# Kernel optimization log

Hardware: AMD Instinct MI355X
Metric: run time of the kernel (lower is better)

The kernel has to match this reference:

```python
import jax, jax.numpy as jnp
import numpy as np
from jax import lax

# --- static config (mirrors cfg / init args) ---
B, T, F_IN = 4, 1024, 80      # batch, time steps, mel bins (80 -> freq collapses to 1)
C_EMB = 512                   # cfg.dim_embed
C0 = C_EMB // 2               # first_conv_filters (non-tcn branch)
HEADS, K = 8, 7               # num_heads, NA kernel_size (dilation=1)
D_HEAD = C_EMB // HEADS
MLP = 4 * C_EMB               # mlp_ratio=4
EPS = 1e-5                    # layer_norm_eps


def setup_inputs() -> dict:
    key = jax.random.key(0)
    ks = jax.random.split(key, 16)
    rn = lambda k, s, sc=0.02: jax.random.normal(k, s, dtype=jnp.float32) * sc
    z = lambda *s: jnp.zeros(s, dtype=jnp.float32)
    o = lambda *s: jnp.ones(s, dtype=jnp.float32)
    return {
        "x": jax.random.normal(ks[0], (B, 1, T, F_IN), dtype=jnp.float32),
        # conv embedding stack (OIHW)
        "conv0_w": rn(ks[1], (C0, 1, 3, 3), 0.1), "conv0_b": z(C0),
        "conv1_w": rn(ks[2], (C_EMB, C0, 1, 12), 0.02), "conv1_b": z(C_EMB),
        "conv2_w": rn(ks[3], (C_EMB, C_EMB, 3, 3), 0.02), "conv2_b": z(C_EMB),
        "emb_ln_g": o(C_EMB), "emb_ln_b": z(C_EMB),
        # neighborhood attention (linear weights stored [in,out]; apply as x @ W + b)
        "q_w": rn(ks[4], (C_EMB, C_EMB)), "q_b": z(C_EMB),
        "k_w": rn(ks[5], (C_EMB, C_EMB)), "k_b": z(C_EMB),
        "v_w": rn(ks[6], (C_EMB, C_EMB)), "v_b": z(C_EMB),
        "rpb": rn(ks[7], (HEADS, 2 * K - 1)),
        "attn_out_w": rn(ks[8], (C_EMB, C_EMB)), "attn_out_b": z(C_EMB),
        "ln1_g": o(C_EMB), "ln1_b": z(C_EMB),
        "ln2_g": o(C_EMB), "ln2_b": z(C_EMB),
        "mlp1_w": rn(ks[9], (C_EMB, MLP)), "mlp1_b": z(MLP),
        "mlp2_w": rn(ks[10], (MLP, C_EMB)), "mlp2_b": z(C_EMB),
    }


def _layer_norm(x, g, b):
    m = jnp.mean(x, axis=-1, keepdims=True)
    v = jnp.mean(jnp.square(x - m), axis=-1, keepdims=True)
    return (x - m) * lax.rsqrt(v + EPS) * g + b


def _na1d(q, k, v, rpb):
    """1D neighborhood attention (natten1dqkrpb + softmax + natten1dav), dilation=1.
    q,k,v: [B,H,T,D]; rpb: [H,2K-1]. Returns [B,H,T,D]."""
    Bq, H, Tq, D = q.shape
    ni = jnp.clip(jnp.arange(Tq) - K // 2, 0, Tq - K)        # window start per query
    idx = ni[:, None] + jnp.arange(K)                         # [T,K] key positions
    k_win = k[:, :, idx]                                      # [B,H,T,K,D]
    v_win = v[:, :, idx]                                      # [B,H,T,K,D]
    scores = jnp.einsum('bhtd,bhtkd->bhtk', q, k_win)
    rel = idx - jnp.arange(Tq)[:, None] + (K - 1)             # [T,K] in [0,2K-2]
    scores = scores + rpb[:, rel][None]                       # + [1,H,T,K]
    probs = jax.nn.softmax(scores, axis=-1)
    return jnp.einsum('bhtk,bhtkd->bhtd', probs, v_win)


def _forward(x, conv0_w, conv0_b, conv1_w, conv1_b, conv2_w, conv2_b,
             emb_ln_g, emb_ln_b, q_w, q_b, k_w, k_b, v_w, v_b, rpb,
             attn_out_w, attn_out_b, ln1_g, ln1_b, ln2_g, ln2_b,
             mlp1_w, mlp1_b, mlp2_w, mlp2_b):
    conv = lambda h, w, b, pad: lax.conv_general_dilated(
        h, w, (1, 1), pad, dimension_numbers=('NCHW', 'OIHW', 'NCHW')
    ) + b[None, :, None, None]
    pool3 = lambda h: lax.reduce_window(h, -jnp.inf, lax.max,
                                        (1, 1, 1, 3), (1, 1, 1, 3), 'VALID')
    # --- AllInOneEmbeddings (eval: dropouts are no-ops) ---
    h = jax.nn.relu(pool3(conv(x, conv0_w, conv0_b, [(1, 1), (0, 0)])))
    h = jax.nn.relu(pool3(conv(h, conv1_w, conv1_b, [(0, 0), (0, 0)])))
    h = jax.nn.relu(pool3(conv(h, conv2_w, conv2_b, [(1, 1), (0, 0)])))
    h = jnp.transpose(h[..., 0], (0, 2, 1))                   # [B,T,C]
    emb = _layer_norm(h, emb_ln_g, emb_ln_b)
    # --- DinatLayer1d (double_attention=False, drop_path=0) ---
    Bh, Th, Ch = emb.shape
    shortcut = emb
    hs = _layer_norm(emb, ln1_g, ln1_b)
    heads = lambda y: jnp.transpose(y.reshape(Bh, Th, HEADS, D_HEAD), (0, 2, 1, 3))
    q = heads(hs @ q_w + q_b) * (1.0 / jnp.sqrt(jnp.float32(D_HEAD)))
    kk = heads(hs @ k_w + k_b)
    vv = heads(hs @ v_w + v_b)
    ctx = _na1d(q, kk, vv, rpb)                               # [B,H,T,D]
    ctx = jnp.transpose(ctx, (0, 2, 1, 3)).reshape(Bh, Th, Ch)
    attn = ctx @ attn_out_w + attn_out_b                      # NeighborhoodAttentionOutput
    hs = shortcut + attn
    ln = _layer_norm(hs, ln2_g, ln2_b)
    mlp = jax.nn.gelu(ln @ mlp1_w + mlp1_b, approximate=False) @ mlp2_w + mlp2_b
    return hs + mlp


def reference(x, conv0_w, conv0_b, conv1_w, conv1_b, conv2_w, conv2_b,
              emb_ln_g, emb_ln_b, q_w, q_b, k_w, k_b, v_w, v_b, rpb,
              attn_out_w, attn_out_b, ln1_g, ln1_b, ln2_g, ln2_b,
              mlp1_w, mlp1_b, mlp2_w, mlp2_b):
    return _forward(x, conv0_w, conv0_b, conv1_w, conv1_b, conv2_w, conv2_b,
                    emb_ln_g, emb_ln_b, q_w, q_b, k_w, k_b, v_w, v_b, rpb,
                    attn_out_w, attn_out_b, ln1_g, ln1_b, ln2_g, ln2_b,
                    mlp1_w, mlp1_b, mlp2_w, mlp2_b)
```

## Files before the change

kernel.cpp:

```cpp
#include <hip/hip_runtime.h>
#include <hip/hip_bf16.h>
#include <math.h>


typedef __bf16 bf16x8 __attribute__((ext_vector_type(8)));
typedef float f32x4 __attribute__((ext_vector_type(4)));

static __device__ __forceinline__ short f2bf(float f) {
  __hip_bfloat16 h = __float2bfloat16(f);
  return __builtin_bit_cast(short, h);
}

static __device__ __forceinline__ float wave_sum(float v) {
#pragma unroll
  for (int o = 32; o; o >>= 1) v += __shfl_xor(v, o);
  return v;
}

static __device__ __forceinline__ void gld16(const void* g, void* l) {
  __builtin_amdgcn_global_load_lds(
      (const __attribute__((address_space(1))) unsigned int*)g,
      (__attribute__((address_space(3))) unsigned int*)l, 16, 0, 0);
}

__global__ __launch_bounds__(256) void conv0_kernel(
    const float* __restrict__ x, const float* __restrict__ w,
    const float* __restrict__ bias, short* __restrict__ h0) {
  const int b = blockIdx.x >> 10;
  const int t = blockIdx.x & 1023;
  const int c = threadIdx.x;
  __shared__ float xs[3][80];
  for (int i = threadIdx.x; i < 240; i += 256) {
    int dt = i / 80, f = i - dt * 80;
    int tt = t + dt - 1;
    xs[dt][f] = (tt >= 0 && tt < 1024) ? x[(b * 1024 + tt) * 80 + f] : 0.f;
  }
  float wr[9];
#pragma unroll
  for (int i = 0; i < 9; ++i) wr[i] = w[c * 9 + i];
  const float bi = bias[c];
  __syncthreads();
  const int cc = c >> 5, q = (c >> 3) & 3, e = c & 7;
  short* outb = &h0[((size_t)(b * 8 + cc) * 1024 + t) * 896];
  for (int fo = 0; fo < 26; ++fo) {
    float m = -1e30f;
#pragma unroll
    for (int p = 0; p < 3; ++p) {
      const int f = fo * 3 + p;
      float acc = bi;
#pragma unroll
      for (int dt = 0; dt < 3; ++dt)
#pragma unroll
        for (int df = 0; df < 3; ++df)
          acc += xs[dt][f + df] * wr[dt * 3 + df];
      m = fmaxf(m, acc);
    }
    const int row = t * 28 + fo;
    outb[fo * 32 + (q ^ ((row >> 1) & 3)) * 8 + e] = f2bf(fmaxf(m, 0.f));
  }
  if (c < 64) outb[832 + c] = 0;
}

__global__ __launch_bounds__(256) void prep_w1(const float* __restrict__ w,
                                               short* __restrict__ wt) {
  const int co = blockIdx.x;
  __shared__ float ls[3072];
  for (int i = threadIdx.x; i < 3072; i += 256) ls[i] = w[co * 3072 + i];
  __syncthreads();
  const int swz = (co >> 1) & 3;
  for (int i = threadIdx.x; i < 3072; i += 256) {
    const int e = i & 7, q = (i >> 3) & 3, kw = (i >> 5) % 12, cc = i / 384;
    const int ci = cc * 32 + q * 8 + e;
    wt[(((size_t)(cc * 12 + kw) * 512 + co) * 4 + (q ^ swz)) * 8 + e] =
        f2bf(ls[ci * 12 + kw]);
  }
}

__global__ __launch_bounds__(256) void prep_w2(const float* __restrict__ w,
                                               short* __restrict__ wt) {
  const int co = blockIdx.x;
  __shared__ float ls[4608];
  for (int i = threadIdx.x; i < 4608; i += 256) ls[i] = w[co * 4608 + i];
  __syncthreads();
  const int swz = (co >> 1) & 3;
  for (int i = threadIdx.x; i < 4608; i += 256) {
    const int e = i & 7, q = (i >> 3) & 3, p = (i >> 5) % 9, cc = i / 288;
    const int ci = cc * 32 + q * 8 + e;
    wt[(((size_t)(cc * 9 + p) * 512 + co) * 4 + (q ^ swz)) * 8 + e] =
        f2bf(ls[ci * 9 + p]);
  }
}

__global__ void prep_wt(const float* __restrict__ w, short* __restrict__ wt,
                        int K, int N) {
  __shared__ float tile[32][33];
  const int k0 = blockIdx.x * 32, n0 = blockIdx.y * 32;
  const int tx = threadIdx.x, ty = threadIdx.y;
  for (int r = ty; r < 32; r += 8) tile[r][tx] = w[(size_t)(k0 + r) * N + n0 + tx];
  __syncthreads();
  for (int r = ty; r < 32; r += 8) wt[(size_t)(n0 + r) * K + k0 + tx] = f2bf(tile[tx][r]);
}

__global__ __launch_bounds__(256) void zero_h1_edges(short* __restrict__ h1) {
  short* base = h1 + (size_t)blockIdx.x * 164160;
  for (int i = threadIdx.x; i < 160; i += 256) {
    base[i] = 0;
    base[1025 * 160 + i] = 0;
  }
}

__global__ __launch_bounds__(512) void conv1_kernel(
    const short* __restrict__ h0, const short* __restrict__ wt1,
    const float* __restrict__ bias, short* __restrict__ h1) {
  const int b = blockIdx.x >> 5;
  const int t0 = (blockIdx.x & 31) * 32;
  const int co0 = blockIdx.y * 128;
  __shared__ short XsF[2][28672];
  __shared__ short AsF[2][8192];
  const int tid = threadIdx.x;
  const int lane = tid & 63;
  const int wid = tid >> 6;
  const int wm = wid >> 2;
  const int wn = wid & 3;
  const int l15 = lane & 15, lg = lane >> 4;

  const f32x4 zf = {0.f, 0.f, 0.f, 0.f};
  f32x4 acc[4][8];
#pragma unroll
  for (int i = 0; i < 4; ++i)
#pragma unroll
    for (int j = 0; j < 8; ++j) acc[i][j] = zf;

  auto stageX = [&](int cc, int buf) {
    const short* xs = h0 + ((size_t)(b * 8 + cc) * 1024 + t0) * 896;
#pragma unroll
    for (int i = 0; i < 7; ++i) {
      const int v = wid * 7 + i;
      gld16(xs + v * 512 + lane * 8, &XsF[buf][v * 512]);
    }
  };
  auto stageA = [&](int cc, int g, int buf) {
#pragma unroll
    for (int i = 0; i < 2; ++i) {
      const int u = wid * 2 + i;
      const int kwl = u >> 3, r = u & 7;
      gld16(wt1 + ((size_t)((cc * 12 + g * 2 + kwl) * 512) + co0) * 32 +
                r * 512 + lane * 8,
            &AsF[buf][kwl * 4096 + r * 512]);
    }
  };

  stageX(0, 0);
  stageA(0, 0, 0);
  asm volatile("s_waitcnt vmcnt(0)" ::: "memory");
  __builtin_amdgcn_s_barrier();

  for (int s = 0; s < 48; ++s) {
    const int cc = s / 6, g = s - cc * 6;
    if (s < 47) {
      const int s1 = s + 1;
      const int cc1 = s1 / 6, g1 = s1 - cc1 * 6;
      stageA(cc1, g1, s1 & 1);
      if (g1 == 0) {
        stageX(cc1, cc1 & 1);
        asm volatile("s_waitcnt vmcnt(9)" ::: "memory");
      } else {
        asm volatile("s_waitcnt vmcnt(2)" ::: "memory");
      }
    } else {
      asm volatile("s_waitcnt vmcnt(0)" ::: "memory");
    }
    __builtin_amdgcn_s_barrier();
    const short* Xb = XsF[cc & 1];
    const short* Ab = AsF[s & 1];
#pragma unroll
    for (int j = 0; j < 2; ++j) {
      const int kw = g * 2 + j;
      bf16x8 a[4];
#pragma unroll
      for (int sm = 0; sm < 4; ++sm) {
        const int co_l = wm * 64 + sm * 16 + l15;
        a[sm] = *reinterpret_cast<const bf16x8*>(
            &Ab[(j * 512 + co_l * 4 + (lg ^ ((co_l >> 1) & 3))) * 8]);
      }
#pragma unroll
      for (int sn = 0; sn < 8; ++sn) {
        const int row = (wn * 8 + sn) * 28 + l15 + kw;
        bf16x8 bf = *reinterpret_cast<const bf16x8*>(
            &Xb[(row * 4 + (lg ^ ((row >> 1) & 3))) * 8]);
#pragma unroll
        for (int sm = 0; sm < 4; ++sm)
          acc[sm][sn] = __builtin_amdgcn_mfma_f32_16x16x32_bf16(a[sm], bf, acc[sm][sn], 0, 0, 0);
      }
    }
    asm volatile("" ::: "memory");
    __builtin_amdgcn_s_barrier();
  }
  const int basel = lane & 48;
  const int wsrc = (l15 < 5) ? 3 * l15 : 0;
#pragma unroll
  for (int sm = 0; sm < 4; ++sm)
#pragma unroll
    for (int sn = 0; sn < 8; ++sn) {
      const int t = t0 + wn * 8 + sn;
#pragma unroll
      for (int r = 0; r < 4; ++r) {
        float val = acc[sm][sn][r];
        float v0 = __shfl(val, basel + wsrc);
        float v1 = __shfl(val, basel + wsrc + 1);
        float v2 = __shfl(val, basel + wsrc + 2);
        if (l15 < 5) {
          const int co = co0 + wm * 64 + sm * 16 + lg * 4 + r;
          float p = fmaxf(fmaxf(v0, v1), v2) + bias[co];
          const int cc2 = co >> 5, q = (co >> 3) & 3, e = co & 7;
          const int row_g = (t + 1) * 5 + l15;
          h1[((size_t)(b * 16 + cc2) * 1026 + (t + 1)) * 160 + l15 * 32 +
             (q ^ ((row_g >> 1) & 3)) * 8 + e] = f2bf(fmaxf(p, 0.f));
        }
      }
    }
}

__global__ __launch_bounds__(512) void conv2_kernel(
    const short* __restrict__ h1, const short* __restrict__ wt2,
    const float* __restrict__ bias, float* __restrict__ emb_in) {
  const int b = blockIdx.x >> 5;
  const int t0 = (blockIdx.x & 31) * 32;
  const int co0 = blockIdx.y * 128;
  __shared__ __align__(16) short smem2[35840];
  const int tid = threadIdx.x;
  const int lane = tid & 63;
  const int wid = tid >> 6;
  const int wm = wid >> 1;
  const int wn = wid & 1;
  const int l15 = lane & 15, lg = lane >> 4;
  const f32x4 zf = {0.f, 0.f, 0.f, 0.f};
  f32x4 acc[2][3];
#pragma unroll
  for (int i = 0; i < 2; ++i)
#pragma unroll
    for (int j = 0; j < 3; ++j) acc[i][j] = zf;
  int tl[3], dwl[3];
#pragma unroll
  for (int sn = 0; sn < 3; ++sn) {
    const int c = wn * 48 + sn * 16 + l15;
    tl[sn] = c / 3;
    dwl[sn] = c - tl[sn] * 3;
  }

  auto stageX = [&](int cc, int buf) {
    const short* xs = h1 + ((size_t)(b * 16 + cc) * 1026 + t0) * 160;
#pragma unroll
    for (int i = 0; i < 2; ++i) {
      const int v = wid + 8 * i;
      if (v < 11) gld16(xs + v * 512 + lane * 8, &smem2[buf * 5632 + v * 512]);
    }
  };
  auto stageA = [&](int cc, int g, int buf) {
#pragma unroll
    for (int i = 0; i < 3; ++i) {
      const int u = wid * 3 + i;
      const int pl = u >> 3, r = u & 7;
      gld16(wt2 + ((size_t)((cc * 9 + g * 3 + pl) * 512) + co0) * 32 +
                r * 512 + lane * 8,
            &smem2[11264 + buf * 12288 + pl * 4096 + r * 512]);
    }
  };

  stageX(0, 0);
  stageA(0, 0, 0);
  asm volatile("s_waitcnt vmcnt(0)" ::: "memory");
  __builtin_amdgcn_s_barrier();

  for (int s = 0; s < 48; ++s) {
    const int cc = s / 3, g = s - cc * 3;
    if (s < 47) {
      const int s1 = s + 1;
      const int cc1 = s1 / 3, g1 = s1 - cc1 * 3;
      stageA(cc1, g1, s1 & 1);
      if (g1 == 0) {
        stageX(cc1, cc1 & 1);
        if (wid < 3) asm volatile("s_waitcnt vmcnt(5)" ::: "memory");
        else         asm volatile("s_waitcnt vmcnt(4)" ::: "memory");
      } else {
        asm volatile("s_waitcnt vmcnt(3)" ::: "memory");
      }
    } else {
      asm volatile("s_waitcnt vmcnt(0)" ::: "memory");
    }
    __builtin_amdgcn_s_barrier();
    const short* Xb = &smem2[(cc & 1) * 5632];
    const short* Ab = &smem2[11264 + (s & 1) * 12288];
#pragma unroll
    for (int j = 0; j < 3; ++j) {
      bf16x8 a[2];
#pragma unroll
      for (int sm = 0; sm < 2; ++sm) {
        const int co_l = wm * 32 + sm * 16 + l15;
        a[sm] = *reinterpret_cast<const bf16x8*>(
            &Ab[(j * 512 + co_l * 4 + (lg ^ ((co_l >> 1) & 3))) * 8]);
      }
#pragma unroll
      for (int sn = 0; sn < 3; ++sn) {
        const int row = (tl[sn] + g) * 5 + dwl[sn] + j;
        bf16x8 xv = *reinterpret_cast<const bf16x8*>(
            &Xb[(row * 4 + (lg ^ ((row >> 1) & 3))) * 8]);
#pragma unroll
        for (int sm = 0; sm < 2; ++sm)
          acc[sm][sn] = __builtin_amdgcn_mfma_f32_16x16x32_bf16(a[sm], xv, acc[sm][sn], 0, 0, 0);
      }
    }
    asm volatile("" ::: "memory");
    __builtin_amdgcn_s_barrier();
  }
  float(*Ds)[100] = reinterpret_cast<float(*)[100]>(smem2);
#pragma unroll
  for (int sm = 0; sm < 2; ++sm)
#pragma unroll
    for (int sn = 0; sn < 3; ++sn)
#pragma unroll
      for (int r = 0; r < 4; ++r)
        Ds[wm * 32 + sm * 16 + lg * 4 + r][wn * 48 + sn * 16 + l15] = acc[sm][sn][r];
  __syncthreads();
  for (int e = tid; e < 4096; e += 512) {
    const int co = e & 127, tt = e >> 7;
    float m = fmaxf(fmaxf(Ds[co][tt * 3], Ds[co][tt * 3 + 1]), Ds[co][tt * 3 + 2]) + bias[co0 + co];
    emb_in[((size_t)(b * 1024) + t0 + tt) * 512 + co0 + co] = fmaxf(m, 0.f);
  }
}

__global__ __launch_bounds__(256) void ln_double_kernel(
    const float* __restrict__ x, const float* __restrict__ g0,
    const float* __restrict__ b0, const float* __restrict__ g1,
    const float* __restrict__ b1, float* __restrict__ o0, float* __restrict__ o1) {
  const int row = blockIdx.x * 4 + (threadIdx.x >> 6);
  const int lane = threadIdx.x & 63;
  const float* xr = x + (size_t)row * 512;
  float v[8];
#pragma unroll
  for (int j = 0; j < 8; ++j) v[j] = xr[j * 64 + lane];
  float s = 0;
#pragma unroll
  for (int j = 0; j < 8; ++j) s += v[j];
  s = wave_sum(s);
  const float mean = s * (1.f / 512.f);
  float q = 0;
#pragma unroll
  for (int j = 0; j < 8; ++j) { float d = v[j] - mean; q += d * d; }
  q = wave_sum(q);
  const float rs = rsqrtf(q * (1.f / 512.f) + 1e-5f);
#pragma unroll
  for (int j = 0; j < 8; ++j) {
    const int ci = j * 64 + lane;
    float e = (v[j] - mean) * rs * g0[ci] + b0[ci];
    o0[(size_t)row * 512 + ci] = e;
    v[j] = e;
  }
  s = 0;
#pragma unroll
  for (int j = 0; j < 8; ++j) s += v[j];
  s = wave_sum(s);
  const float mean2 = s * (1.f / 512.f);
  q = 0;
#pragma unroll
  for (int j = 0; j < 8; ++j) { float d = v[j] - mean2; q += d * d; }
  q = wave_sum(q);
  const float rs2 = rsqrtf(q * (1.f / 512.f) + 1e-5f);
#pragma unroll
  for (int j = 0; j < 8; ++j) {
    const int ci = j * 64 + lane;
    o1[(size_t)row * 512 + ci] = (v[j] - mean2) * rs2 * g1[ci] + b1[ci];
  }
}

__global__ __launch_bounds__(256) void ln_kernel(
    const float* __restrict__ x, const float* __restrict__ g,
    const float* __restrict__ b, float* __restrict__ o) {
  const int row = blockIdx.x * 4 + (threadIdx.x >> 6);
  const int lane = threadIdx.x & 63;
  const float* xr = x + (size_t)row * 512;
  float v[8];
#pragma unroll
  for (int j = 0; j < 8; ++j) v[j] = xr[j * 64 + lane];
  float s = 0;
#pragma unroll
  for (int j = 0; j < 8; ++j) s += v[j];
  s = wave_sum(s);
  const float mean = s * (1.f / 512.f);
  float q = 0;
#pragma unroll
  for (int j = 0; j < 8; ++j) { float d = v[j] - mean; q += d * d; }
  q = wave_sum(q);
  const float rs = rsqrtf(q * (1.f / 512.f) + 1e-5f);
#pragma unroll
  for (int j = 0; j < 8; ++j) {
    const int ci = j * 64 + lane;
    o[(size_t)row * 512 + ci] = (v[j] - mean) * rs * g[ci] + b[ci];
  }
}

__global__ __launch_bounds__(256) void na1d_kernel(
    const float* __restrict__ q, const float* __restrict__ k,
    const float* __restrict__ v, const float* __restrict__ rpb,
    float* __restrict__ ctx) {
  const int W = blockIdx.x * 4 + (threadIdx.x >> 6);
  const int lane = threadIdx.x & 63;
  const int b = W >> 13, h = (W >> 10) & 7, t = W & 1023;
  int ni = t - 3;
  ni = ni < 0 ? 0 : (ni > 1017 ? 1017 : ni);
  const size_t base = (size_t)(b * 1024) * 512 + h * 64;
  const float qv = q[base + (size_t)t * 512 + lane];
  const float* kb = k + base + (size_t)ni * 512;
  float s[7];
#pragma unroll
  for (int j = 0; j < 7; ++j) {
    float pd = qv * kb[j * 512 + lane];
    pd = wave_sum(pd);
    s[j] = pd + rpb[h * 13 + (ni + j - t + 6)];
  }
  float mx = s[0];
#pragma unroll
  for (int j = 1; j < 7; ++j) mx = fmaxf(mx, s[j]);
  float den = 0;
#pragma unroll
  for (int j = 0; j < 7; ++j) { s[j] = expf(s[j] - mx); den += s[j]; }
  const float inv = 1.f / den;
  const float* vb = v + base + (size_t)ni * 512;
  float o = 0;
#pragma unroll
  for (int j = 0; j < 7; ++j) o += s[j] * vb[j * 512 + lane];
  ctx[base + (size_t)t * 512 + lane] = o * inv;
}

template <int EPI>
__global__ __launch_bounds__(256) void gemm_tf(
    const float* __restrict__ A, const short* __restrict__ Wt,
    const float* __restrict__ bias, const float* __restrict__ res,
    float* __restrict__ C, int K, int N) {
  const int m0 = blockIdx.x * 128, n0 = blockIdx.y * 64;
  __shared__ short Asm[128][40];
  __shared__ short Bsm[64][40];
  const int tid = threadIdx.x;
  const int wid = tid >> 6, lane = tid & 63;
  const int wm = wid >> 1, wn = wid & 1;
  const int l15 = lane & 15, lg = lane >> 4;
  const f32x4 zf = {0.f, 0.f, 0.f, 0.f};
  f32x4 acc[4][2];
#pragma unroll
  for (int i = 0; i < 4; ++i) { acc[i][0] = zf; acc[i][1] = zf; }
  const int ar = tid >> 1, ahf = (tid & 1) * 16;
  for (int k0 = 0; k0 < K; k0 += 32) {
    __syncthreads();
    {
      const float4* s = reinterpret_cast<const float4*>(&A[(size_t)(m0 + ar) * K + k0 + ahf]);
      float4 f0 = s[0], f1 = s[1], f2 = s[2], f3 = s[3];
      short* d = &Asm[ar][ahf];
      d[0] = f2bf(f0.x);  d[1] = f2bf(f0.y);  d[2] = f2bf(f0.z);  d[3] = f2bf(f0.w);
      d[4] = f2bf(f1.x);  d[5] = f2bf(f1.y);  d[6] = f2bf(f1.z);  d[7] = f2bf(f1.w);
      d[8] = f2bf(f2.x);  d[9] = f2bf(f2.y);  d[10] = f2bf(f2.z); d[11] = f2bf(f2.w);
      d[12] = f2bf(f3.x); d[13] = f2bf(f3.y); d[14] = f2bf(f3.z); d[15] = f2bf(f3.w);
    }
    if (tid < 128) {
      const int br = tid >> 1, bhf = (tid & 1) * 16;
      const int4* s = reinterpret_cast<const int4*>(&Wt[(size_t)(n0 + br) * K + k0 + bhf]);
      int4* d = reinterpret_cast<int4*>(&Bsm[br][bhf]);
      d[0] = s[0];
      d[1] = s[1];
    }
    __syncthreads();
    bf16x8 bfr[2];
#pragma unroll
    for (int sn = 0; sn < 2; ++sn)
      bfr[sn] = *reinterpret_cast<const bf16x8*>(&Bsm[wn * 32 + sn * 16 + l15][lg * 8]);
#pragma unroll
    for (int sm = 0; sm < 4; ++sm) {
      bf16x8 a = *reinterpret_cast<const bf16x8*>(&Asm[wm * 64 + sm * 16 + l15][lg * 8]);
#pragma unroll
      for (int sn = 0; sn < 2; ++sn)
        acc[sm][sn] = __builtin_amdgcn_mfma_f32_16x16x32_bf16(a, bfr[sn], acc[sm][sn], 0, 0, 0);
    }
  }
#pragma unroll
  for (int sm = 0; sm < 4; ++sm)
#pragma unroll
    for (int sn = 0; sn < 2; ++sn)
#pragma unroll
      for (int r = 0; r < 4; ++r) {
        const int m = m0 + wm * 64 + sm * 16 + lg * 4 + r;
        const int n = n0 + wn * 32 + sn * 16 + l15;
        float val = acc[sm][sn][r] + bias[n];
        if (EPI == 1) val *= 0.125f;
        if (EPI == 2) val = 0.5f * val * (1.f + erff(val * 0.70710678f));
        if (EPI == 3) val += res[(size_t)m * N + n];
        C[(size_t)m * N + n] = val;
      }
}

extern "C" void kernel_launch(void* const* d_in, const int* in_sizes, int n_in,
                              void* d_out, int out_size, void* d_ws, size_t ws_size,
                              hipStream_t stream) {
  (void)in_sizes; (void)n_in; (void)out_size;
  const float* x        = (const float*)d_in[0];
  const float* conv0_w  = (const float*)d_in[1];
  const float* conv0_b  = (const float*)d_in[2];
  const float* conv1_w  = (const float*)d_in[3];
  const float* conv1_b  = (const float*)d_in[4];
  const float* conv2_w  = (const float*)d_in[5];
  const float* conv2_b  = (const float*)d_in[6];
  const float* emb_ln_g = (const float*)d_in[7];
  const float* emb_ln_b = (const float*)d_in[8];
  const float* q_w  = (const float*)d_in[9];
  const float* q_b  = (const float*)d_in[10];
  const float* k_w  = (const float*)d_in[11];
  const float* k_b  = (const float*)d_in[12];
  const float* v_w  = (const float*)d_in[13];
  const float* v_b  = (const float*)d_in[14];
  const float* rpb  = (const float*)d_in[15];
  const float* ao_w = (const float*)d_in[16];
  const float* ao_b = (const float*)d_in[17];
  const float* ln1_g = (const float*)d_in[18];
  const float* ln1_b = (const float*)d_in[19];
  const float* ln2_g = (const float*)d_in[20];
  const float* ln2_b = (const float*)d_in[21];
  const float* m1_w = (const float*)d_in[22];
  const float* m1_b = (const float*)d_in[23];
  const float* m2_w = (const float*)d_in[24];
  const float* m2_b = (const float*)d_in[25];

  char* ws = (char*)d_ws;
  size_t off = 0;
  auto alloc = [&](size_t bytes) -> char* {
    char* p = ws + off;
    off += (bytes + 255) & ~(size_t)255;
    return p;
  };
  short* h0   = (short*)alloc(4ull * 8 * 1024 * 896 * 2);
  short* h1   = (short*)alloc(4ull * 16 * 1026 * 160 * 2);
  float* embi = (float*)alloc(4ull * 1024 * 512 * 4);
  float* emb  = (float*)alloc(4ull * 1024 * 512 * 4);
  float* hs1  = (float*)alloc(4ull * 1024 * 512 * 4);
  float* qb   = (float*)alloc(4ull * 1024 * 512 * 4);
  float* kb   = (float*)alloc(4ull * 1024 * 512 * 4);
  float* vb   = (float*)alloc(4ull * 1024 * 512 * 4);
  float* ctx  = (float*)alloc(4ull * 1024 * 512 * 4);
  float* hs   = (float*)alloc(4ull * 1024 * 512 * 4);
  short* wt1  = (short*)alloc(512ull * 12 * 256 * 2);
  short* wt2  = (short*)alloc(512ull * 9 * 512 * 2);
  short* wtq  = (short*)alloc(512ull * 512 * 2);
  short* wtk  = (short*)alloc(512ull * 512 * 2);
  short* wtv  = (short*)alloc(512ull * 512 * 2);
  short* wtao = (short*)alloc(512ull * 512 * 2);
  short* wtm1 = (short*)alloc(2048ull * 512 * 2);
  short* wtm2 = (short*)alloc(512ull * 2048 * 2);
  if (ws_size < off) return;
  float* mid  = (float*)h0;
  float* ln2o = embi;
  float* outp = (float*)d_out;

  prep_w1<<<512, 256, 0, stream>>>(conv1_w, wt1);
  prep_w2<<<512, 256, 0, stream>>>(conv2_w, wt2);
  zero_h1_edges<<<64, 256, 0, stream>>>(h1);
  dim3 tb(32, 8);
  prep_wt<<<dim3(16, 16), tb, 0, stream>>>(q_w, wtq, 512, 512);
  prep_wt<<<dim3(16, 16), tb, 0, stream>>>(k_w, wtk, 512, 512);
  prep_wt<<<dim3(16, 16), tb, 0, stream>>>(v_w, wtv, 512, 512);
  prep_wt<<<dim3(16, 16), tb, 0, stream>>>(ao_w, wtao, 512, 512);
  prep_wt<<<dim3(16, 64), tb, 0, stream>>>(m1_w, wtm1, 512, 2048);
  prep_wt<<<dim3(64, 16), tb, 0, stream>>>(m2_w, wtm2, 2048, 512);

  conv0_kernel<<<4096, 256, 0, stream>>>(x, conv0_w, conv0_b, h0);
  conv1_kernel<<<dim3(128, 4), 512, 0, stream>>>(h0, wt1, conv1_b, h1);
  conv2_kernel<<<dim3(128, 4), 512, 0, stream>>>(h1, wt2, conv2_b, embi);
  ln_double_kernel<<<1024, 256, 0, stream>>>(embi, emb_ln_g, emb_ln_b, ln1_g, ln1_b, emb, hs1);
  gemm_tf<1><<<dim3(32, 8), 256, 0, stream>>>(hs1, wtq, q_b, nullptr, qb, 512, 512);
  gemm_tf<0><<<dim3(32, 8), 256, 0, stream>>>(hs1, wtk, k_b, nullptr, kb, 512, 512);
  gemm_tf<0><<<dim3(32, 8), 256, 0, stream>>>(hs1, wtv, v_b, nullptr, vb, 512, 512);
  na1d_kernel<<<8192, 256, 0, stream>>>(qb, kb, vb, rpb, ctx);
  gemm_tf<3><<<dim3(32, 8), 256, 0, stream>>>(ctx, wtao, ao_b, emb, hs, 512, 512);
  ln_kernel<<<1024, 256, 0, stream>>>(hs, ln2_g, ln2_b, ln2o);
  gemm_tf<2><<<dim3(32, 32), 256, 0, stream>>>(ln2o, wtm1, m1_b, nullptr, mid, 512, 2048);
  gemm_tf<3><<<dim3(32, 8), 256, 0, stream>>>(mid, wtm2, m2_b, hs, outp, 2048, 512);
}
```

Baseline: 499.5 us.

## Fuse QKV GEMMs, store GEMM inputs in bf16, double-buffer GEMM via LDS-direct loads

```diff
diff --git a/kernel.cpp b/kernel.cpp
--- a/kernel.cpp
+++ b/kernel.cpp
@@ -9,6 +9,11 @@
 static __device__ __forceinline__ short f2bf(float f) {
   __hip_bfloat16 h = __float2bfloat16(f);
   return __builtin_bit_cast(short, h);
+}
+
+static __device__ __forceinline__ float bf2f(short s) {
+  unsigned int u = ((unsigned int)(unsigned short)s) << 16;
+  return __builtin_bit_cast(float, u);
 }
 
 static __device__ __forceinline__ float wave_sum(float v) {
@@ -107,6 +112,13 @@
     base[i] = 0;
     base[1025 * 160 + i] = 0;
   }
+}
+
+__global__ __launch_bounds__(256) void concat3_kernel(
+    const float* __restrict__ a, const float* __restrict__ b,
+    const float* __restrict__ c, float* __restrict__ o) {
+  const int i = blockIdx.x * 256 + threadIdx.x;
+  o[i] = i < 512 ? a[i] : (i < 1024 ? b[i - 512] : c[i - 1024]);
 }
 
 __global__ __launch_bounds__(512) void conv1_kernel(
@@ -332,7 +344,7 @@
 __global__ __launch_bounds__(256) void ln_double_kernel(
     const float* __restrict__ x, const float* __restrict__ g0,
     const float* __restrict__ b0, const float* __restrict__ g1,
-    const float* __restrict__ b1, float* __restrict__ o0, float* __restrict__ o1) {
+    const float* __restrict__ b1, float* __restrict__ o0, short* __restrict__ o1) {
   const int row = blockIdx.x * 4 + (threadIdx.x >> 6);
   const int lane = threadIdx.x & 63;
   const float* xr = x + (size_t)row * 512;
@@ -369,13 +381,13 @@
 #pragma unroll
   for (int j = 0; j < 8; ++j) {
     const int ci = j * 64 + lane;
-    o1[(size_t)row * 512 + ci] = (v[j] - mean2) * rs2 * g1[ci] + b1[ci];
+    o1[(size_t)row * 512 + ci] = f2bf((v[j] - mean2) * rs2 * g1[ci] + b1[ci]);
   }
 }
 
 __global__ __launch_bounds__(256) void ln_kernel(
     const float* __restrict__ x, const float* __restrict__ g,
-    const float* __restrict__ b, float* __restrict__ o) {
+    const float* __restrict__ b, short* __restrict__ o) {
   const int row = blockIdx.x * 4 + (threadIdx.x >> 6);
   const int lane = threadIdx.x & 63;
   const float* xr = x + (size_t)row * 512;
@@ -395,26 +407,24 @@
 #pragma unroll
   for (int j = 0; j < 8; ++j) {
     const int ci = j * 64 + lane;
-    o[(size_t)row * 512 + ci] = (v[j] - mean) * rs * g[ci] + b[ci];
+    o[(size_t)row * 512 + ci] = f2bf((v[j] - mean) * rs * g[ci] + b[ci]);
   }
 }
 
 __global__ __launch_bounds__(256) void na1d_kernel(
-    const float* __restrict__ q, const float* __restrict__ k,
-    const float* __restrict__ v, const float* __restrict__ rpb,
-    float* __restrict__ ctx) {
+    const float* __restrict__ qkv, const float* __restrict__ rpb,
+    short* __restrict__ ctx) {
   const int W = blockIdx.x * 4 + (threadIdx.x >> 6);
   const int lane = threadIdx.x & 63;
   const int b = W >> 13, h = (W >> 10) & 7, t = W & 1023;
   int ni = t - 3;
   ni = ni < 0 ? 0 : (ni > 1017 ? 1017 : ni);
-  const size_t base = (size_t)(b * 1024) * 512 + h * 64;
-  const float qv = q[base + (size_t)t * 512 + lane];
-  const float* kb = k + base + (size_t)ni * 512;
+  const float qv = qkv[((size_t)(b * 1024) + t) * 1536 + h * 64 + lane];
+  const float* kb = qkv + 512 + ((size_t)(b * 1024) + ni) * 1536 + h * 64;
   float s[7];
 #pragma unroll
   for (int j = 0; j < 7; ++j) {
-    float pd = qv * kb[j * 512 + lane];
+    float pd = qv * kb[j * 1536 + lane];
     pd = wave_sum(pd);
     s[j] = pd + rpb[h * 13 + (ni + j - t + 6)];
   }
@@ -425,60 +435,80 @@
 #pragma unroll
   for (int j = 0; j < 7; ++j) { s[j] = expf(s[j] - mx); den += s[j]; }
   const float inv = 1.f / den;
-  const float* vb = v + base + (size_t)ni * 512;
+  const float* vb = qkv + 1024 + ((size_t)(b * 1024) + ni) * 1536 + h * 64;
   float o = 0;
 #pragma unroll
-  for (int j = 0; j < 7; ++j) o += s[j] * vb[j * 512 + lane];
-  ctx[base + (size_t)t * 512 + lane] = o * inv;
+  for (int j = 0; j < 7; ++j) o += s[j] * vb[j * 1536 + lane];
+  ctx[((size_t)(b * 1024) + t) * 512 + h * 64 + lane] = f2bf(o * inv);
 }
 
 template <int EPI>
-__global__ __launch_bounds__(256) void gemm_tf(
-    const float* __restrict__ A, const short* __restrict__ Wt,
+__global__ __launch_bounds__(256) void gemm_bf(
+    const short* __restrict__ A, const short* __restrict__ Wt,
     const float* __restrict__ bias, const float* __restrict__ res,
-    float* __restrict__ C, int K, int N) {
+    void* __restrict__ Cv, int K, int N) {
   const int m0 = blockIdx.x * 128, n0 = blockIdx.y * 64;
-  __shared__ short Asm[128][40];
-  __shared__ short Bsm[64][40];
+  __shared__ short Asm[2][8192];
+  __shared__ short Bsm[2][4096];
   const int tid = threadIdx.x;
   const int wid = tid >> 6, lane = tid & 63;
   const int wm = wid >> 1, wn = wid & 1;
   const int l15 = lane & 15, lg = lane >> 4;
+  const int srow = lane >> 3, su = lane & 7;
+  const int ssw = (su ^ srow) << 3;
   const f32x4 zf = {0.f, 0.f, 0.f, 0.f};
   f32x4 acc[4][2];
 #pragma unroll
   for (int i = 0; i < 4; ++i) { acc[i][0] = zf; acc[i][1] = zf; }
-  const int ar = tid >> 1, ahf = (tid & 1) * 16;
-  for (int k0 = 0; k0 < K; k0 += 32) {
-    __syncthreads();
-    {
-      const float4* s = reinterpret_cast<const float4*>(&A[(size_t)(m0 + ar) * K + k0 + ahf]);
-      float4 f0 = s[0], f1 = s[1], f2 = s[2], f3 = s[3];
-      short* d = &Asm[ar][ahf];
-      d[0] = f2bf(f0.x);  d[1] = f2bf(f0.y);  d[2] = f2bf(f0.z);  d[3] = f2bf(f0.w);
-      d[4] = f2bf(f1.x);  d[5] = f2bf(f1.y);  d[6] = f2bf(f1.z);  d[7] = f2bf(f1.w);
-      d[8] = f2bf(f2.x);  d[9] = f2bf(f2.y);  d[10] = f2bf(f2.z); d[11] = f2bf(f2.w);
-      d[12] = f2bf(f3.x); d[13] = f2bf(f3.y); d[14] = f2bf(f3.z); d[15] = f2bf(f3.w);
-    }
-    if (tid < 128) {
-      const int br = tid >> 1, bhf = (tid & 1) * 16;
-      const int4* s = reinterpret_cast<const int4*>(&Wt[(size_t)(n0 + br) * K + k0 + bhf]);
-      int4* d = reinterpret_cast<int4*>(&Bsm[br][bhf]);
-      d[0] = s[0];
-      d[1] = s[1];
-    }
-    __syncthreads();
-    bf16x8 bfr[2];
-#pragma unroll
-    for (int sn = 0; sn < 2; ++sn)
-      bfr[sn] = *reinterpret_cast<const bf16x8*>(&Bsm[wn * 32 + sn * 16 + l15][lg * 8]);
-#pragma unroll
-    for (int sm = 0; sm < 4; ++sm) {
-      bf16x8 a = *reinterpret_cast<const bf16x8*>(&Asm[wm * 64 + sm * 16 + l15][lg * 8]);
-#pragma unroll
-      for (int sn = 0; sn < 2; ++sn)
-        acc[sm][sn] = __builtin_amdgcn_mfma_f32_16x16x32_bf16(a, bfr[sn], acc[sm][sn], 0, 0, 0);
-    }
+
+  auto stage = [&](int k0, int buf) {
+#pragma unroll
+    for (int i = 0; i < 4; ++i) {
+      const int r0 = (wid * 4 + i) * 8;
+      gld16(A + (size_t)(m0 + r0 + srow) * K + k0 + ssw, &Asm[buf][r0 * 64]);
+    }
+#pragma unroll
+    for (int i = 0; i < 2; ++i) {
+      const int r0 = (wid * 2 + i) * 8;
+      gld16(Wt + (size_t)(n0 + r0 + srow) * K + k0 + ssw, &Bsm[buf][r0 * 64]);
+    }
+  };
+
+  const int S = K >> 6;
+  stage(0, 0);
+  asm volatile("s_waitcnt vmcnt(0)" ::: "memory");
+  __builtin_amdgcn_s_barrier();
+
+  for (int s = 0; s < S; ++s) {
+    if (s < S - 1) {
+      stage((s + 1) << 6, (s + 1) & 1);
+      asm volatile("s_waitcnt vmcnt(6)" ::: "memory");
+    } else {
+      asm volatile("s_waitcnt vmcnt(0)" ::: "memory");
+    }
+    __builtin_amdgcn_s_barrier();
+    const short* Ab = Asm[s & 1];
+    const short* Bb = Bsm[s & 1];
+#pragma unroll
+    for (int kk = 0; kk < 2; ++kk) {
+      const int u = kk * 4 + lg;
+      bf16x8 bfr[2];
+#pragma unroll
+      for (int sn = 0; sn < 2; ++sn) {
+        const int rn = wn * 32 + sn * 16 + l15;
+        bfr[sn] = *reinterpret_cast<const bf16x8*>(&Bb[rn * 64 + ((u ^ (rn & 7)) << 3)]);
+      }
+#pragma unroll
+      for (int sm = 0; sm < 4; ++sm) {
+        const int rm = wm * 64 + sm * 16 + l15;
+        bf16x8 a = *reinterpret_cast<const bf16x8*>(&Ab[rm * 64 + ((u ^ (rm & 7)) << 3)]);
+#pragma unroll
+        for (int sn = 0; sn < 2; ++sn)
+          acc[sm][sn] = __builtin_amdgcn_mfma_f32_16x16x32_bf16(a, bfr[sn], acc[sm][sn], 0, 0, 0);
+      }
+    }
+    asm volatile("" ::: "memory");
+    __builtin_amdgcn_s_barrier();
   }
 #pragma unroll
   for (int sm = 0; sm < 4; ++sm)
@@ -489,10 +519,14 @@
         const int m = m0 + wm * 64 + sm * 16 + lg * 4 + r;
         const int n = n0 + wn * 32 + sn * 16 + l15;
         float val = acc[sm][sn][r] + bias[n];
-        if (EPI == 1) val *= 0.125f;
-        if (EPI == 2) val = 0.5f * val * (1.f + erff(val * 0.70710678f));
-        if (EPI == 3) val += res[(size_t)m * N + n];
-        C[(size_t)m * N + n] = val;
+        if (EPI == 2) {
+          val = 0.5f * val * (1.f + erff(val * 0.70710678f));
+          ((short*)Cv)[(size_t)m * N + n] = f2bf(val);
+        } else {
+          if (EPI == 3) val += res[(size_t)m * N + n];
+          if (EPI == 4 && n < 512) val *= 0.125f;
+          ((float*)Cv)[(size_t)m * N + n] = val;
+        }
       }
 }
 
@@ -538,32 +572,30 @@
   short* h1   = (short*)alloc(4ull * 16 * 1026 * 160 * 2);
   float* embi = (float*)alloc(4ull * 1024 * 512 * 4);
   float* emb  = (float*)alloc(4ull * 1024 * 512 * 4);
-  float* hs1  = (float*)alloc(4ull * 1024 * 512 * 4);
-  float* qb   = (float*)alloc(4ull * 1024 * 512 * 4);
-  float* kb   = (float*)alloc(4ull * 1024 * 512 * 4);
-  float* vb   = (float*)alloc(4ull * 1024 * 512 * 4);
-  float* ctx  = (float*)alloc(4ull * 1024 * 512 * 4);
+  short* hs1  = (short*)alloc(4ull * 1024 * 512 * 2);
+  float* qkv  = (float*)alloc(4ull * 1024 * 1536 * 4);
+  short* ctx  = (short*)alloc(4ull * 1024 * 512 * 2);
   float* hs   = (float*)alloc(4ull * 1024 * 512 * 4);
   short* wt1  = (short*)alloc(512ull * 12 * 256 * 2);
   short* wt2  = (short*)alloc(512ull * 9 * 512 * 2);
-  short* wtq  = (short*)alloc(512ull * 512 * 2);
-  short* wtk  = (short*)alloc(512ull * 512 * 2);
-  short* wtv  = (short*)alloc(512ull * 512 * 2);
+  short* wtqkv = (short*)alloc(1536ull * 512 * 2);
   short* wtao = (short*)alloc(512ull * 512 * 2);
   short* wtm1 = (short*)alloc(2048ull * 512 * 2);
   short* wtm2 = (short*)alloc(512ull * 2048 * 2);
+  float* qkvb = (float*)alloc(1536ull * 4);
   if (ws_size < off) return;
-  float* mid  = (float*)h0;
-  float* ln2o = embi;
+  short* mid  = (short*)h0;
+  short* ln2o = (short*)embi;
   float* outp = (float*)d_out;
 
   prep_w1<<<512, 256, 0, stream>>>(conv1_w, wt1);
   prep_w2<<<512, 256, 0, stream>>>(conv2_w, wt2);
   zero_h1_edges<<<64, 256, 0, stream>>>(h1);
+  concat3_kernel<<<6, 256, 0, stream>>>(q_b, k_b, v_b, qkvb);
   dim3 tb(32, 8);
-  prep_wt<<<dim3(16, 16), tb, 0, stream>>>(q_w, wtq, 512, 512);
-  prep_wt<<<dim3(16, 16), tb, 0, stream>>>(k_w, wtk, 512, 512);
-  prep_wt<<<dim3(16, 16), tb, 0, stream>>>(v_w, wtv, 512, 512);
+  prep_wt<<<dim3(16, 16), tb, 0, stream>>>(q_w, wtqkv, 512, 512);
+  prep_wt<<<dim3(16, 16), tb, 0, stream>>>(k_w, wtqkv + 512 * 512, 512, 512);
+  prep_wt<<<dim3(16, 16), tb, 0, stream>>>(v_w, wtqkv + 1024 * 512, 512, 512);
   prep_wt<<<dim3(16, 16), tb, 0, stream>>>(ao_w, wtao, 512, 512);
   prep_wt<<<dim3(16, 64), tb, 0, stream>>>(m1_w, wtm1, 512, 2048);
   prep_wt<<<dim3(64, 16), tb, 0, stream>>>(m2_w, wtm2, 2048, 512);
@@ -572,12 +604,10 @@
   conv1_kernel<<<dim3(128, 4), 512, 0, stream>>>(h0, wt1, conv1_b, h1);
   conv2_kernel<<<dim3(128, 4), 512, 0, stream>>>(h1, wt2, conv2_b, embi);
   ln_double_kernel<<<1024, 256, 0, stream>>>(embi, emb_ln_g, emb_ln_b, ln1_g, ln1_b, emb, hs1);
-  gemm_tf<1><<<dim3(32, 8), 256, 0, stream>>>(hs1, wtq, q_b, nullptr, qb, 512, 512);
-  gemm_tf<0><<<dim3(32, 8), 256, 0, stream>>>(hs1, wtk, k_b, nullptr, kb, 512, 512);
-  gemm_tf<0><<<dim3(32, 8), 256, 0, stream>>>(hs1, wtv, v_b, nullptr, vb, 512, 512);
-  na1d_kernel<<<8192, 256, 0, stream>>>(qb, kb, vb, rpb, ctx);
-  gemm_tf<3><<<dim3(32, 8), 256, 0, stream>>>(ctx, wtao, ao_b, emb, hs, 512, 512);
+  gemm_bf<4><<<dim3(32, 24), 256, 0, stream>>>(hs1, wtqkv, qkvb, nullptr, qkv, 512, 1536);
+  na1d_kernel<<<8192, 256, 0, stream>>>(qkv, rpb, ctx);
+  gemm_bf<3><<<dim3(32, 8), 256, 0, stream>>>(ctx, wtao, ao_b, emb, hs, 512, 512);
   ln_kernel<<<1024, 256, 0, stream>>>(hs, ln2_g, ln2_b, ln2o);
-  gemm_tf<2><<<dim3(32, 32), 256, 0, stream>>>(ln2o, wtm1, m1_b, nullptr, mid, 512, 2048);
-  gemm_tf<3><<<dim3(32, 8), 256, 0, stream>>>(mid, wtm2, m2_b, hs, outp, 2048, 512);
-}
+  gemm_bf<2><<<dim3(32, 32), 256, 0, stream>>>(ln2o, wtm1, m1_b, nullptr, mid, 512, 2048);
+  gemm_bf<3><<<dim3(32, 8), 256, 0, stream>>>(mid, wtm2, m2_b, hs, outp, 2048, 512);
+}
```

After: 417.6 us. 1.2x faster.
